# Performance work log

Hardware: AMD Instinct MI355X
Metric: run time of the kernel (lower is better)

## Reference

```python
import jax, jax.numpy as jnp
import numpy as np

V, K, F = 150000, 32, 96


def setup_inputs() -> dict:
    key = jax.random.key(0)
    k1, k2 = jax.random.split(key)
    feat = jax.random.normal(k1, (V, F), dtype=jnp.float32)
    nidx = jax.random.randint(k2, (V, K), 0, V, dtype=jnp.int64)
    return {"feat": feat, "nidx": nidx}


def reference(feat, nidx):
    # AccumulateNeighbours(mode='meanmax') with zero distances and all-valid
    # neighbor indices: AccumulateKnn weights exp(-10*0)=1, and the appended
    # ones-column normalization in AccumulateKnnSumw divides by K/K = 1.
    # => output = [mean over K neighbors, max over K neighbors], shape [V, 2F]
    neigh = feat[nidx]                 # gather: [V, K, F]
    fmean = jnp.mean(neigh, axis=1)    # [V, F]
    fmax = jnp.max(neigh, axis=1)      # [V, F]
    return jnp.concatenate([fmean, fmax], axis=1)  # [V, 2F]
```

## Files before the change

kernel.cpp:

```cpp
#include <hip/hip_runtime.h>
#include <math.h>
#include <stdint.h>


constexpr int V = 150000;
constexpr int K = 32;
constexpr int F = 96;

typedef float f32x4 __attribute__((ext_vector_type(4)));
typedef int   i32x4 __attribute__((ext_vector_type(4)));

constexpr int AB_BLOCKS = 1024;

__global__ __launch_bounds__(256)
void absmax_partial(const f32x4* __restrict__ in, int n4, float* __restrict__ partial)
{
    __shared__ float lm[4];
    float m = 0.f;
    for (int i = blockIdx.x * 256 + threadIdx.x; i < n4; i += AB_BLOCKS * 256) {
        f32x4 x = __builtin_nontemporal_load(&in[i]);
        m = fmaxf(m, fmaxf(fmaxf(fabsf(x.x), fabsf(x.y)),
                           fmaxf(fabsf(x.z), fabsf(x.w))));
    }
    #pragma unroll
    for (int off = 32; off > 0; off >>= 1)
        m = fmaxf(m, __shfl_down(m, off));
    if ((threadIdx.x & 63) == 0) lm[threadIdx.x >> 6] = m;
    __syncthreads();
    if (threadIdx.x == 0)
        partial[blockIdx.x] = fmaxf(fmaxf(lm[0], lm[1]), fmaxf(lm[2], lm[3]));
}

__global__ __launch_bounds__(256)
void quantize_i8(const f32x4* __restrict__ feat4,
                 const float* __restrict__ partial,
                 float*       __restrict__ amax_out,
                 unsigned*    __restrict__ q32, int nq)
{
    __shared__ float lm[4];
    __shared__ float samax;
    float m = 0.f;
    for (int j = threadIdx.x; j < AB_BLOCKS; j += 256)
        m = fmaxf(m, partial[j]);
    #pragma unroll
    for (int off = 32; off > 0; off >>= 1)
        m = fmaxf(m, __shfl_down(m, off));
    if ((threadIdx.x & 63) == 0) lm[threadIdx.x >> 6] = m;
    __syncthreads();
    if (threadIdx.x == 0)
        samax = fmaxf(fmaxf(lm[0], lm[1]), fmaxf(lm[2], lm[3]));
    __syncthreads();

    const float amax = samax;
    const float inv  = amax > 0.f ? 127.f / amax : 0.f;

    const int i = blockIdx.x * 256 + threadIdx.x;
    if (i < nq) {
        f32x4 x = __builtin_nontemporal_load(&feat4[i]);
        const int b0 = (int)rintf(fminf(fmaxf(x.x * inv, -127.f), 127.f));
        const int b1 = (int)rintf(fminf(fmaxf(x.y * inv, -127.f), 127.f));
        const int b2 = (int)rintf(fminf(fmaxf(x.z * inv, -127.f), 127.f));
        const int b3 = (int)rintf(fminf(fmaxf(x.w * inv, -127.f), 127.f));
        const unsigned p = (unsigned)(b0 & 0xff)
                         | ((unsigned)(b1 & 0xff) << 8)
                         | ((unsigned)(b2 & 0xff) << 16)
                         | ((unsigned)(b3 & 0xff) << 24);
        __builtin_nontemporal_store(p, &q32[i]);
    }
    if (blockIdx.x == 0 && threadIdx.x == 0) *amax_out = amax;
}

constexpr int CI   = F / 16;
constexpr int VBI  = 32;
constexpr int BLKI = VBI * CI;
constexpr int SSTR = K + 1;
constexpr int NB   = 16;
constexpr int BROWS = (V + NB - 1) / NB;
constexpr int CSTR = NB + 1;

__global__ __launch_bounds__(BLKI)
void accum_meanmax_i8(const uint4* __restrict__ q4,
                      const int*   __restrict__ nidx,
                      const float* __restrict__ amaxp,
                      float*       __restrict__ out)
{
    __shared__ int sraw[VBI * SSTR];
    __shared__ int ssrt[VBI * SSTR];
    __shared__ int scnt[VBI * CSTR];

    const int tid   = threadIdx.x;
    const int vbase = blockIdx.x * VBI;

    {
        const i32x4* n4p = reinterpret_cast<const i32x4*>(nidx + (size_t)vbase * K);
        for (int j = tid; j < VBI * K / 4; j += BLKI) {
            const int l  = j << 2;
            const int vl = l >> 5;
            const int k  = l & (K - 1);
            if (vbase + vl < V) {
                i32x4 w = __builtin_nontemporal_load(&n4p[j]);
                int* dst = &sraw[vl * SSTR + k];
                dst[0] = w.x; dst[1] = w.y; dst[2] = w.z; dst[3] = w.w;
            }
        }
        for (int j = tid; j < VBI * CSTR; j += BLKI)
            scnt[j] = 0;
    }
    __syncthreads();

    if (tid < VBI && vbase + tid < V) {
        const int* r   = &sraw[tid * SSTR];
        int*       cnt = &scnt[tid * CSTR];
        #pragma unroll 8
        for (int k = 0; k < K; ++k)
            cnt[r[k] / BROWS] += 1;
        int run = 0;
        #pragma unroll
        for (int c = 0; c < NB; ++c) { run += cnt[c]; cnt[c] = run; }
        int* s = &ssrt[tid * SSTR];
        #pragma unroll 8
        for (int k = 0; k < K; ++k) {
            const int n = r[k];
            s[--cnt[n / BROWS]] = n;
        }
    }
    __syncthreads();

    const int vl = tid / CI;
    const int c  = tid % CI;
    const int v  = vbase + vl;
    if (v >= V) return;

    const int* my = &ssrt[vl * SSTR];

    int sum[16], mx[16];
    #pragma unroll
    for (int j = 0; j < 16; ++j) { sum[j] = 0; mx[j] = -128; }

    #pragma unroll 8
    for (int k = 0; k < K; ++k) {
        const int n = my[k];
        const uint4 raw = q4[(size_t)n * CI + c];
        const unsigned w[4] = { raw.x, raw.y, raw.z, raw.w };
        #pragma unroll
        for (int j = 0; j < 4; ++j) {
            #pragma unroll
            for (int t = 0; t < 4; ++t) {
                const int x = (int)(int8_t)(w[j] >> (8 * t));
                sum[4 * j + t] += x;
                mx[4 * j + t]   = x > mx[4 * j + t] ? x : mx[4 * j + t];
            }
        }
    }

    const float sc  = *amaxp * (1.f / 127.f);
    const float msc = sc * (1.f / (float)K);

    f32x4* o4 = reinterpret_cast<f32x4*>(out + (size_t)v * (2 * F));
    #pragma unroll
    for (int j = 0; j < 4; ++j) {
        f32x4 mn = { sum[4*j]   * msc, sum[4*j+1] * msc,
                     sum[4*j+2] * msc, sum[4*j+3] * msc };
        f32x4 mg = { mx[4*j]   * sc, mx[4*j+1] * sc,
                     mx[4*j+2] * sc, mx[4*j+3] * sc };
        o4[4 * c + j]         = mn;
        o4[F / 4 + 4 * c + j] = mg;
    }
}

constexpr int CF   = F / 4;
constexpr int VBF  = 8;
constexpr int BLKF = VBF * CF;

__global__ __launch_bounds__(BLKF)
void accum_meanmax_f32(const float4* __restrict__ feat4,
                       const int*    __restrict__ nidx,
                       float4*       __restrict__ out4)
{
    __shared__ int sidx[VBF * K];
    const int tid   = threadIdx.x;
    const int vbase = blockIdx.x * VBF;
    for (int i = tid; i < VBF * K; i += BLKF)
        sidx[i] = nidx[vbase * K + i];
    __syncthreads();

    const int vl = tid / CF;
    const int c  = tid % CF;
    const int v  = vbase + vl;

    float4 s = make_float4(0.f, 0.f, 0.f, 0.f);
    float4 m = make_float4(-INFINITY, -INFINITY, -INFINITY, -INFINITY);
    const int* my_idx = &sidx[vl * K];

    #pragma unroll 8
    for (int k = 0; k < K; ++k) {
        const int n = my_idx[k];
        const float4 x = feat4[n * CF + c];
        s.x += x.x; s.y += x.y; s.z += x.z; s.w += x.w;
        m.x = fmaxf(m.x, x.x); m.y = fmaxf(m.y, x.y);
        m.z = fmaxf(m.z, x.z); m.w = fmaxf(m.w, x.w);
    }
    const float inv = 1.0f / (float)K;
    out4[v * (2 * CF) + c]      = make_float4(s.x * inv, s.y * inv, s.z * inv, s.w * inv);
    out4[v * (2 * CF) + CF + c] = m;
}

extern "C" void kernel_launch(void* const* d_in, const int* in_sizes, int n_in,
                              void* d_out, int out_size, void* d_ws, size_t ws_size,
                              hipStream_t stream) {
    const float* feat = (const float*)d_in[0];
    const int*   nidx = (const int*)d_in[1];
    float*       out  = (float*)d_out;

    const size_t tab_bytes = (size_t)V * F;
    const size_t need = 8192 + tab_bytes;

    if (ws_size >= need) {
        float*    partial = (float*)d_ws;
        float*    amax    = (float*)((char*)d_ws + 4096);
        unsigned* q32     = (unsigned*)((char*)d_ws + 8192);

        const int n4 = V * F / 4;
        absmax_partial<<<AB_BLOCKS, 256, 0, stream>>>((const f32x4*)feat, n4, partial);

        const int nq = V * (F / 4);
        quantize_i8<<<(nq + 255) / 256, 256, 0, stream>>>(
            (const f32x4*)feat, partial, amax, q32, nq);

        const int Gt = (V + VBI - 1) / VBI;
        accum_meanmax_i8<<<Gt, BLKI, 0, stream>>>(
            (const uint4*)q32, nidx, amax, out);
    } else {
        accum_meanmax_f32<<<V / VBF, BLKF, 0, stream>>>(
            (const float4*)feat, (const int*)nidx, (float4*)out);
    }
}
```

Measured before the change: 259.6 us.

## Presort neighbor indices in absmax pass and process two vertices per thread

Each vertex's 32 neighbor indices are fully sorted with an in-register bitonic network inside the absmax reduction kernel and written to a workspace buffer. The gather kernel no longer does its own shared-memory bucket sort. Each thread now accumulates two vertices, so more independent gathers are in flight, and sorted indices should give better locality for the int8 table lookups. The cost is an extra index buffer written and read back, more register pressure, and a larger workspace; the old in-kernel-sort path is kept as a fallback.

```diff
diff --git a/kernel.cpp b/kernel.cpp
--- a/kernel.cpp
+++ b/kernel.cpp
@@ -13,11 +13,16 @@
 constexpr int AB_BLOCKS = 1024;
 
 __global__ __launch_bounds__(256)
-void absmax_partial(const f32x4* __restrict__ in, int n4, float* __restrict__ partial)
+void absmax_sort(const f32x4* __restrict__ in, int n4,
+                 float* __restrict__ partial,
+                 const int* __restrict__ nidx,
+                 int*       __restrict__ nsrt)
 {
     __shared__ float lm[4];
+    const int gid = blockIdx.x * 256 + threadIdx.x;
+
     float m = 0.f;
-    for (int i = blockIdx.x * 256 + threadIdx.x; i < n4; i += AB_BLOCKS * 256) {
+    for (int i = gid; i < n4; i += AB_BLOCKS * 256) {
         f32x4 x = __builtin_nontemporal_load(&in[i]);
         m = fmaxf(m, fmaxf(fmaxf(fabsf(x.x), fabsf(x.y)),
                            fmaxf(fabsf(x.z), fabsf(x.w))));
@@ -29,6 +34,37 @@
     __syncthreads();
     if (threadIdx.x == 0)
         partial[blockIdx.x] = fmaxf(fmaxf(lm[0], lm[1]), fmaxf(lm[2], lm[3]));
+
+    if (nsrt != nullptr && gid < V) {
+        int n[K];
+        const i32x4* src = reinterpret_cast<const i32x4*>(nidx + (size_t)gid * K);
+        #pragma unroll
+        for (int j = 0; j < K / 4; ++j) {
+            i32x4 w = __builtin_nontemporal_load(&src[j]);
+            n[4*j] = w.x; n[4*j+1] = w.y; n[4*j+2] = w.z; n[4*j+3] = w.w;
+        }
+        #pragma unroll
+        for (int k = 2; k <= K; k <<= 1) {
+            #pragma unroll
+            for (int j = k >> 1; j > 0; j >>= 1) {
+                #pragma unroll
+                for (int i = 0; i < K; ++i) {
+                    const int l = i ^ j;
+                    if (l > i) {
+                        const int a = n[i], b = n[l];
+                        if ((i & k) == 0) { n[i] = min(a, b); n[l] = max(a, b); }
+                        else              { n[i] = max(a, b); n[l] = min(a, b); }
+                    }
+                }
+            }
+        }
+        i32x4* dst = reinterpret_cast<i32x4*>(nsrt + (size_t)gid * K);
+        #pragma unroll
+        for (int j = 0; j < K / 4; ++j) {
+            i32x4 w = { n[4*j], n[4*j+1], n[4*j+2], n[4*j+3] };
+            __builtin_nontemporal_store(w, &dst[j]);
+        }
+    }
 }
 
 __global__ __launch_bounds__(256)
@@ -71,29 +107,118 @@
 }
 
 constexpr int CI   = F / 16;
-constexpr int VBI  = 32;
-constexpr int BLKI = VBI * CI;
+constexpr int VBI  = 64;
+constexpr int BLKI = 192;
 constexpr int SSTR = K + 1;
+
+__global__ __launch_bounds__(BLKI)
+void accum_meanmax_i8(const uint4* __restrict__ q4,
+                      const int*   __restrict__ nsrt,
+                      const float* __restrict__ amaxp,
+                      float*       __restrict__ out)
+{
+    __shared__ int sidx[VBI * SSTR];
+
+    const int tid   = threadIdx.x;
+    const int vbase = blockIdx.x * VBI;
+
+    {
+        const i32x4* n4p = reinterpret_cast<const i32x4*>(nsrt + (size_t)vbase * K);
+        for (int j = tid; j < VBI * K / 4; j += BLKI) {
+            const int l  = j << 2;
+            const int vl = l >> 5;
+            const int k  = l & (K - 1);
+            if (vbase + vl < V) {
+                i32x4 w = __builtin_nontemporal_load(&n4p[j]);
+                int* dst = &sidx[vl * SSTR + k];
+                dst[0] = w.x; dst[1] = w.y; dst[2] = w.z; dst[3] = w.w;
+            }
+        }
+    }
+    __syncthreads();
+
+    const int vl = tid / CI;
+    const int c  = tid % CI;
+    const int v0 = vbase + vl;
+    const int v1 = vbase + 32 + vl;
+    if (v0 >= V) return;
+
+    const int* my0 = &sidx[vl * SSTR];
+    const int* my1 = (v1 < V) ? &sidx[(vl + 32) * SSTR] : my0;
+
+    int s0[16], m0[16], s1[16], m1[16];
+    #pragma unroll
+    for (int j = 0; j < 16; ++j) { s0[j] = 0; m0[j] = -128; s1[j] = 0; m1[j] = -128; }
+
+    #pragma unroll 4
+    for (int k = 0; k < K; ++k) {
+        const int   na = my0[k];
+        const int   nb = my1[k];
+        const uint4 ra = q4[(size_t)na * CI + c];
+        const uint4 rb = q4[(size_t)nb * CI + c];
+        const unsigned wa[4] = { ra.x, ra.y, ra.z, ra.w };
+        const unsigned wb[4] = { rb.x, rb.y, rb.z, rb.w };
+        #pragma unroll
+        for (int j = 0; j < 4; ++j) {
+            #pragma unroll
+            for (int t = 0; t < 4; ++t) {
+                const int xa = (int)(int8_t)(wa[j] >> (8 * t));
+                const int xb = (int)(int8_t)(wb[j] >> (8 * t));
+                s0[4*j+t] += xa;
+                m0[4*j+t]  = xa > m0[4*j+t] ? xa : m0[4*j+t];
+                s1[4*j+t] += xb;
+                m1[4*j+t]  = xb > m1[4*j+t] ? xb : m1[4*j+t];
+            }
+        }
+    }
+
+    const float sc  = *amaxp * (1.f / 127.f);
+    const float msc = sc * (1.f / (float)K);
+
+    {
+        f32x4* o4 = reinterpret_cast<f32x4*>(out + (size_t)v0 * (2 * F));
+        #pragma unroll
+        for (int j = 0; j < 4; ++j) {
+            f32x4 mn = { s0[4*j]*msc, s0[4*j+1]*msc, s0[4*j+2]*msc, s0[4*j+3]*msc };
+            f32x4 mg = { m0[4*j]*sc,  m0[4*j+1]*sc,  m0[4*j+2]*sc,  m0[4*j+3]*sc  };
+            o4[4 * c + j]         = mn;
+            o4[F / 4 + 4 * c + j] = mg;
+        }
+    }
+    if (v1 < V) {
+        f32x4* o4 = reinterpret_cast<f32x4*>(out + (size_t)v1 * (2 * F));
+        #pragma unroll
+        for (int j = 0; j < 4; ++j) {
+            f32x4 mn = { s1[4*j]*msc, s1[4*j+1]*msc, s1[4*j+2]*msc, s1[4*j+3]*msc };
+            f32x4 mg = { m1[4*j]*sc,  m1[4*j+1]*sc,  m1[4*j+2]*sc,  m1[4*j+3]*sc  };
+            o4[4 * c + j]         = mn;
+            o4[F / 4 + 4 * c + j] = mg;
+        }
+    }
+}
+
+constexpr int VB5  = 32;
+constexpr int BLK5 = VB5 * CI;
 constexpr int NB   = 16;
 constexpr int BROWS = (V + NB - 1) / NB;
 constexpr int CSTR = NB + 1;
 
-__global__ __launch_bounds__(BLKI)
-void accum_meanmax_i8(const uint4* __restrict__ q4,
-                      const int*   __restrict__ nidx,
-                      const float* __restrict__ amaxp,
-                      float*       __restrict__ out)
-{
-    __shared__ int sraw[VBI * SSTR];
-    __shared__ int ssrt[VBI * SSTR];
-    __shared__ int scnt[VBI * CSTR];
+__global__ __launch_bounds__(BLK5)
+void accum_meanmax_i8_insort(const uint4* __restrict__ q4,
+                             const int*   __restrict__ nidx,
+                             const float* __restrict__ amaxp,
+                             float*       __restrict__ out)
+{
+    __shared__ int sraw[VB5 * SSTR];
+    __shared__ int ssrt[VB5 * SSTR];
+    __shared__ int scnt[VB5 * CSTR];
 
     const int tid   = threadIdx.x;
-    const int vbase = blockIdx.x * VBI;
+    const int vbase = blockIdx.x * VB5;
 
     {
         const i32x4* n4p = reinterpret_cast<const i32x4*>(nidx + (size_t)vbase * K);
-        for (int j = tid; j < VBI * K / 4; j += BLKI) {
+        for (int j = tid; j < VB5 * K / 4; j += BLK5) {
             const int l  = j << 2;
             const int vl = l >> 5;
             const int k  = l & (K - 1);
@@ -103,12 +228,12 @@
                 dst[0] = w.x; dst[1] = w.y; dst[2] = w.z; dst[3] = w.w;
             }
         }
-        for (int j = tid; j < VBI * CSTR; j += BLKI)
+        for (int j = tid; j < VB5 * CSTR; j += BLK5)
             scnt[j] = 0;
     }
     __syncthreads();
 
-    if (tid < VBI && vbase + tid < V) {
+    if (tid < VB5 && vbase + tid < V) {
         const int* r   = &sraw[tid * SSTR];
         int*       cnt = &scnt[tid * CSTR];
         #pragma unroll 8
@@ -132,7 +257,6 @@
     if (v >= V) return;
 
     const int* my = &ssrt[vl * SSTR];
-
     int sum[16], mx[16];
     #pragma unroll
     for (int j = 0; j < 16; ++j) { sum[j] = 0; mx[j] = -128; }
@@ -143,26 +267,22 @@
         const uint4 raw = q4[(size_t)n * CI + c];
         const unsigned w[4] = { raw.x, raw.y, raw.z, raw.w };
         #pragma unroll
-        for (int j = 0; j < 4; ++j) {
+        for (int j = 0; j < 4; ++j)
             #pragma unroll
             for (int t = 0; t < 4; ++t) {
                 const int x = (int)(int8_t)(w[j] >> (8 * t));
-                sum[4 * j + t] += x;
-                mx[4 * j + t]   = x > mx[4 * j + t] ? x : mx[4 * j + t];
-            }
-        }
+                sum[4*j+t] += x;
+                mx[4*j+t]   = x > mx[4*j+t] ? x : mx[4*j+t];
+            }
     }
 
     const float sc  = *amaxp * (1.f / 127.f);
     const float msc = sc * (1.f / (float)K);
-
     f32x4* o4 = reinterpret_cast<f32x4*>(out + (size_t)v * (2 * F));
     #pragma unroll
     for (int j = 0; j < 4; ++j) {
-        f32x4 mn = { sum[4*j]   * msc, sum[4*j+1] * msc,
-                     sum[4*j+2] * msc, sum[4*j+3] * msc };
-        f32x4 mg = { mx[4*j]   * sc, mx[4*j+1] * sc,
-                     mx[4*j+2] * sc, mx[4*j+3] * sc };
+        f32x4 mn = { sum[4*j]*msc, sum[4*j+1]*msc, sum[4*j+2]*msc, sum[4*j+3]*msc };
+        f32x4 mg = { mx[4*j]*sc,  mx[4*j+1]*sc,  mx[4*j+2]*sc,  mx[4*j+3]*sc  };
         o4[4 * c + j]         = mn;
         o4[F / 4 + 4 * c + j] = mg;
     }
@@ -212,23 +332,40 @@
     const int*   nidx = (const int*)d_in[1];
     float*       out  = (float*)d_out;
 
-    const size_t tab_bytes = (size_t)V * F;
-    const size_t need = 8192 + tab_bytes;
-
-    if (ws_size >= need) {
+    const size_t tab_bytes  = (size_t)V * F;
+    const size_t sort_bytes = (size_t)V * K * 4;
+    const size_t need_full  = 8192 + tab_bytes + sort_bytes;
+    const size_t need_mid   = 8192 + tab_bytes;
+
+    const int n4 = V * F / 4;
+    const int nq = V * (F / 4);
+
+    if (ws_size >= need_full) {
         float*    partial = (float*)d_ws;
         float*    amax    = (float*)((char*)d_ws + 4096);
         unsigned* q32     = (unsigned*)((char*)d_ws + 8192);
-
-        const int n4 = V * F / 4;
-        absmax_partial<<<AB_BLOCKS, 256, 0, stream>>>((const f32x4*)feat, n4, partial);
-
-        const int nq = V * (F / 4);
+        int*      nsrt    = (int*)((char*)d_ws + 8192 + tab_bytes);
+
+        absmax_sort<<<AB_BLOCKS, 256, 0, stream>>>((const f32x4*)feat, n4,
+                                                   partial, nidx, nsrt);
         quantize_i8<<<(nq + 255) / 256, 256, 0, stream>>>(
             (const f32x4*)feat, partial, amax, q32, nq);
 
         const int Gt = (V + VBI - 1) / VBI;
         accum_meanmax_i8<<<Gt, BLKI, 0, stream>>>(
+            (const uint4*)q32, nsrt, amax, out);
+    } else if (ws_size >= need_mid) {
+        float*    partial = (float*)d_ws;
+        float*    amax    = (float*)((char*)d_ws + 4096);
+        unsigned* q32     = (unsigned*)((char*)d_ws + 8192);
+
+        absmax_sort<<<AB_BLOCKS, 256, 0, stream>>>((const f32x4*)feat, n4,
+                                                   partial, nidx, nullptr);
+        quantize_i8<<<(nq + 255) / 256, 256, 0, stream>>>(
+            (const f32x4*)feat, partial, amax, q32, nq);
+
+        const int Gt = (V + VB5 - 1) / VB5;
+        accum_meanmax_i8_insort<<<Gt, BLK5, 0, stream>>>(
             (const uint4*)q32, nidx, amax, out);
     } else {
         accum_meanmax_f32<<<V / VBF, BLKF, 0, stream>>>(
```

Result: slower. 282.8 us (+9.0%).
